# Kernel optimization log

Measured on AMD Instinct MI355X. Metric: run time of the kernel, lower is better.

Reference implementation:

```python
import jax, jax.numpy as jnp
import numpy as np

B, N, DM = 4, 1024, 256
DEPTH, D_STATE, D_CONV, EXPAND = 12, 16, 4, 2
D_INNER = EXPAND * DM
DT_RANK = (DM + 15) // 16
MASKED = 256            # fixed number of masked tokens per row (CLS never masked)
MAX_VIS = N - MASKED    # static visible length -> jit-safe gather/pad
EPS = 1e-5


def setup_inputs() -> dict:
    key = jax.random.key(0)
    ks = jax.random.split(key, 8)
    tokens = jax.random.normal(ks[0], (B, N, DM), jnp.float32)
    # mask: exactly MASKED random positions True per row, among first N-1 (CLS visible)
    def row_mask(k):
        perm = jax.random.permutation(k, N - 1)
        return jnp.zeros((N,), bool).at[perm[:MASKED]].set(True)
    mask = jax.vmap(row_mask)(jax.random.split(ks[1], B))
    sc = 0.02
    L = DEPTH
    in_proj_w = jax.random.normal(ks[2], (L, 2 * D_INNER, DM), jnp.float32) * sc
    conv_w = jax.random.normal(ks[3], (L, D_INNER, D_CONV), jnp.float32) * sc
    conv_b = jnp.zeros((L, D_INNER), jnp.float32)
    x_proj_w = jax.random.normal(ks[4], (L, DT_RANK + 2 * D_STATE, D_INNER), jnp.float32) * sc
    dt_proj_w = jax.random.normal(ks[5], (L, D_INNER, DT_RANK), jnp.float32) * (DT_RANK ** -0.5)
    dt_proj_b = jnp.full((L, D_INNER), float(np.log(np.expm1(0.01))), jnp.float32)  # softplus^-1(0.01)
    A_log = jnp.log(jnp.broadcast_to(jnp.arange(1, D_STATE + 1, dtype=jnp.float32), (L, D_INNER, D_STATE)))
    D_skip = jnp.ones((L, D_INNER), jnp.float32)
    out_proj_w = jax.random.normal(ks[6], (L, DM, D_INNER), jnp.float32) * sc
    norm_w = jnp.ones((L, DM), jnp.float32)
    norm_f_w = jnp.ones((DM,), jnp.float32)
    ln_w = jnp.ones((DM,), jnp.float32)
    ln_b = jnp.zeros((DM,), jnp.float32)
    return dict(tokens=tokens, mask=mask, in_proj_w=in_proj_w, conv_w=conv_w, conv_b=conv_b,
                x_proj_w=x_proj_w, dt_proj_w=dt_proj_w, dt_proj_b=dt_proj_b, A_log=A_log,
                D_skip=D_skip, out_proj_w=out_proj_w, norm_w=norm_w, norm_f_w=norm_f_w,
                ln_w=ln_w, ln_b=ln_b)


def _rmsnorm(x, w):
    return x * jax.lax.rsqrt(jnp.mean(x * x, axis=-1, keepdims=True) + EPS) * w


def _selective_scan(dA, dBu, C):
    # linear recurrence h_t = dA_t * h_{t-1} + dBu_t via associative scan over time
    def comb(l, r):
        return (r[0] * l[0], r[0] * l[1] + r[1])
    _, h = jax.lax.associative_scan(comb, (dA, dBu), axis=1)  # [B,L,d_inner,d_state]
    return jnp.einsum('blds,bls->bld', h, C)


def _mamba(h, p):
    in_w, cw, cb, xw, dtw, dtb, Alog, Dd, ow = p
    L = h.shape[1]
    xz = jnp.einsum('bld,ed->ble', h, in_w)           # [B,L,2*d_inner]
    x, z = jnp.split(xz, 2, axis=-1)
    # causal depthwise conv1d (torch Conv1d, padding=d_conv-1, truncated to L)
    xp = jnp.pad(x, ((0, 0), (D_CONV - 1, 0), (0, 0)))
    x = sum(xp[:, k:k + L, :] * cw[:, k] for k in range(D_CONV)) + cb
    x = jax.nn.silu(x)
    xdbl = jnp.einsum('bld,ed->ble', x, xw)           # [B,L,dt_rank+2*d_state]
    dtr = xdbl[..., :DT_RANK]
    Bm = xdbl[..., DT_RANK:DT_RANK + D_STATE]
    Cm = xdbl[..., DT_RANK + D_STATE:]
    dt = jax.nn.softplus(jnp.einsum('blr,dr->bld', dtr, dtw) + dtb)  # [B,L,d_inner]
    A = -jnp.exp(Alog)                                 # [d_inner,d_state]
    dA = jnp.exp(dt[..., None] * A)                    # [B,L,d_inner,d_state]
    dBu = (dt * x)[..., None] * Bm[:, :, None, :]
    y = _selective_scan(dA, dBu, Cm) + Dd * x
    y = y * jax.nn.silu(z)
    return jnp.einsum('bld,od->blo', y, ow)


def _forward(tokens, mask, in_proj_w, conv_w, conv_b, x_proj_w, dt_proj_w, dt_proj_b,
             A_log, D_skip, out_proj_w, norm_w, norm_f_w, ln_w, ln_b):
    # gather visible tokens, preserving order (stable sort: visible first)
    sort_key = mask.astype(jnp.int32) * N + jnp.arange(N)
    order = jnp.argsort(sort_key, axis=1)[:, :MAX_VIS]           # [B,MAX_VIS]
    vis = jnp.take_along_axis(tokens, order[..., None], axis=1)  # [B,MAX_VIS,DM]

    def step(carry, p):
        hidden, residual = carry
        residual = hidden + residual
        hidden = _mamba(_rmsnorm(residual, p[0]), p[1:])
        return (hidden, residual), None

    layer_params = (norm_w, in_proj_w, conv_w, conv_b, x_proj_w, dt_proj_w, dt_proj_b,
                    A_log, D_skip, out_proj_w)
    (h, r), _ = jax.lax.scan(step, (vis, jnp.zeros_like(vis)), layer_params)
    h = _rmsnorm(h + r, norm_f_w)
    # final nn.LayerNorm
    mu = jnp.mean(h, axis=-1, keepdims=True)
    var = jnp.mean((h - mu) ** 2, axis=-1, keepdims=True)
    h = (h - mu) * jax.lax.rsqrt(var + EPS) * ln_w + ln_b
    return h[:, :-1], h[:, -1]


def reference(tokens, mask, in_proj_w, conv_w, conv_b, x_proj_w, dt_proj_w, dt_proj_b,
              A_log, D_skip, out_proj_w, norm_w, norm_f_w, ln_w, ln_b):
    return _forward(tokens, mask, in_proj_w, conv_w, conv_b, x_proj_w, dt_proj_w, dt_proj_b,
                    A_log, D_skip, out_proj_w, norm_w, norm_f_w, ln_w, ln_b)
```

## Files before the change

kernel.cpp:

```cpp
#include <hip/hip_runtime.h>
#include <stdint.h>

#define B_ 4
#define N_TOK 1024
#define DM 256
#define DEPTH 12
#define DSTATE 16
#define DIN 512
#define LVIS 768
#define MROWS (B_ * LVIS)
#define NCHUNK 64
#define CLEN 12
#define EPS_F 1e-5f
#define YS 520
#define AS_ 264

typedef __attribute__((ext_vector_type(8))) short s8v;
typedef __attribute__((ext_vector_type(4))) float f4v;

__device__ __forceinline__ float bs2f(uint32_t u) {
  uint32_t x = (u & 0xffffu) << 16;
  float f; __builtin_memcpy(&f, &x, 4); return f;
}
__device__ __forceinline__ uint16_t f2b(float f) {
  uint32_t u; __builtin_memcpy(&u, &f, 4);
  return (uint16_t)((u + 0x7fffu + ((u >> 16) & 1u)) >> 16);
}
__device__ __forceinline__ float silu_f(float x) { return x / (1.f + __expf(-x)); }
__device__ __forceinline__ float softplus_f(float x) {
  return fmaxf(x, 0.f) + log1pf(__expf(-fabsf(x)));
}
__device__ __forceinline__ float block_sum256(float v, volatile float* scr) {
  int t = threadIdx.x, lane = t & 63, wid = t >> 6;
#pragma unroll
  for (int o = 32; o > 0; o >>= 1) v += __shfl_down(v, o);
  __syncthreads();
  if (lane == 0) scr[wid] = v;
  __syncthreads();
  return scr[0] + scr[1] + scr[2] + scr[3];
}

__global__ void detect_kernel(const void* mask, const uint32_t* nf, int* flags) {
  __shared__ int cnt[3];
  int t = threadIdx.x;
  if (t < 3) cnt[t] = 0;
  __syncthreads();
  const uint32_t* pi = (const uint32_t*)mask;
  const uint16_t* ph = (const uint16_t*)mask;
  const uint8_t*  pb = (const uint8_t*)mask;
  int c32 = 0, cbf = 0, c8 = 0;
  for (int i = t; i < 1024; i += 256) {
    c32 += (pi[i] != 0u);
    cbf += (ph[i] != 0);
    c8  += (pb[i] != 0);
  }
  atomicAdd(&cnt[0], c32);
  atomicAdd(&cnt[1], cbf);
  atomicAdd(&cnt[2], c8);
  __syncthreads();
  if (t == 0) {
    int f;
    if (cnt[0] == 256) f = 0;
    else if (cnt[1] == 256) f = 2;
    else f = 1;
    flags[0] = f;
    flags[1] = (nf[0] == 0x3F800000u) ? 0 : 1;
  }
}

struct CvtArgs {
  const void* src[13];
  void*       dst[13];
  int         n[13];
  int         isb16[13];
};
__global__ __launch_bounds__(256) void cvt_all_kernel(CvtArgs a, int total,
                                                      const int* __restrict__ flags) {
  int e = blockIdx.x * 256 + threadIdx.x;
  if (e >= total) return;
  int i = 0;
  while (e >= a.n[i]) { e -= a.n[i]; ++i; }
  int srcb16 = flags[1];
  if (a.isb16[i]) {
    uint16_t v = srcb16 ? ((const uint16_t*)a.src[i])[e]
                        : f2b(((const float*)a.src[i])[e]);
    ((uint16_t*)a.dst[i])[e] = v;
  } else {
    float v = srcb16 ? bs2f(((const uint16_t*)a.src[i])[e])
                     : ((const float*)a.src[i])[e];
    ((float*)a.dst[i])[e] = v;
  }
}

__global__ __launch_bounds__(1024) void order_kernel(const void* mask,
                                                     const int* __restrict__ flags,
                                                     int* __restrict__ order) {
  int b = blockIdx.x, i = threadIdx.x;
  int f = flags[0];
  int mv;
  if (f == 0)      mv = (((const uint32_t*)mask)[b * N_TOK + i] != 0u);
  else if (f == 1) mv = (((const uint8_t*)mask)[b * N_TOK + i] != 0);
  else             mv = (((const uint16_t*)mask)[b * N_TOK + i] != 0);
  int vis = !mv;
  unsigned long long mb = __ballot(vis);
  int lane = i & 63, wid = i >> 6;
  int wpre = __popcll(mb & ((1ull << lane) - 1ull));
  __shared__ int wsum[16];
  __shared__ int woff[16];
  if (lane == 0) wsum[wid] = __popcll(mb);
  __syncthreads();
  if (i == 0) { int a = 0; for (int w = 0; w < 16; ++w) { woff[w] = a; a += wsum[w]; } }
  __syncthreads();
  if (vis) {
    int pos = woff[wid] + wpre;
    if (pos < LVIS) order[b * LVIS + pos] = i;
  }
}

__global__ __launch_bounds__(256) void gather_rms_kernel(const void* __restrict__ tokens,
                                                         const int* __restrict__ order,
                                                         const int* __restrict__ flags,
                                                         const float* __restrict__ nw,
                                                         float* __restrict__ residual,
                                                         uint16_t* __restrict__ rmsb16) {
  __shared__ float scr[4];
  int row = blockIdx.x;
  int b = row / LVIS;
  int d = threadIdx.x;
  int idx = order[row];
  size_t src = ((size_t)(b * N_TOK + idx)) * DM + d;
  float v = flags[1] ? bs2f(((const uint16_t*)tokens)[src]) : ((const float*)tokens)[src];
  size_t i = (size_t)row * DM + d;
  residual[i] = v;
  float ss = block_sum256(v * v, scr);
  rmsb16[i] = f2b(v * rsqrtf(ss / DM + EPS_F) * nw[d]);
}

__device__ __forceinline__ size_t cidx(int b, int c, int s, int d) {
  return (((size_t)(b * NCHUNK + c) * 16 + s)) * DIN + d;
}

__global__ __launch_bounds__(1024, 4) void scan1_kernel(
    const uint16_t* __restrict__ rmsb16, const uint16_t* __restrict__ inw,
    const uint16_t* __restrict__ xw,
    const float* __restrict__ cw, const float* __restrict__ cb,
    const float* __restrict__ dtw, const float* __restrict__ dtb,
    const float* __restrict__ Alog,
    uint16_t* __restrict__ xz16, float* __restrict__ hend,
    float* __restrict__ pend, float* __restrict__ xdbl_out) {
  __shared__ uint16_t As[16 * AS_];
  __shared__ uint16_t xzl[16 * YS];
  __shared__ float red[8][768];
  __shared__ float xds[CLEN * 48];
  const int t = threadIdx.x;
  const int wv = t >> 6, lane = t & 63;
  const int lm = lane & 15, lq = lane >> 4;
  const int c = blockIdx.x & (NCHUNK - 1);
  const int b = blockIdx.x >> 6;
  const int rowbase = b * LVIS + c * CLEN;
  if (t < 512) {
    int r = t >> 5, seg = t & 31;
    int grow = rowbase - 3 + r;
    if (grow < 0) grow = 0;
    if (grow > MROWS - 1) grow = MROWS - 1;
    *(uint4*)(As + r * AS_ + seg * 8) =
        *(const uint4*)(rmsb16 + (size_t)grow * DM + seg * 8);
  }
  __syncthreads();
  {
    f4v acc[4];
#pragma unroll
    for (int j = 0; j < 4; ++j) acc[j] = (f4v){0.f, 0.f, 0.f, 0.f};
    for (int k0 = 0; k0 < DM; k0 += 32) {
      s8v a = *(const s8v*)(As + lm * AS_ + k0 + lq * 8);
#pragma unroll
      for (int j = 0; j < 4; ++j) {
        int n = (4 * wv + j) * 16 + lm;
        s8v bw = *(const s8v*)(inw + (size_t)n * DM + k0 + lq * 8);
        acc[j] = __builtin_amdgcn_mfma_f32_16x16x32_bf16(a, bw, acc[j], 0, 0, 0);
      }
    }
#pragma unroll
    for (int j = 0; j < 4; ++j) {
      int col = (4 * wv + j) * 16 + lm;
#pragma unroll
      for (int rr = 0; rr < 4; ++rr) {
        int tr = lq * 4 + rr;
        uint16_t v = f2b(acc[j][rr]);
        if (col < 512) xzl[tr * YS + col] = v;
        if (tr >= 3 && tr < 15)
          xz16[(size_t)(rowbase + tr - 3) * 1024 + col] = v;
      }
    }
  }
  __syncthreads();
  if (wv < 8) {
    f4v acc[3];
#pragma unroll
    for (int j = 0; j < 3; ++j) acc[j] = (f4v){0.f, 0.f, 0.f, 0.f};
    const int l = c * CLEN + lm;
    const bool t3 = l >= 3, t2 = l >= 2, t1 = l >= 1;
#pragma unroll
    for (int ki = 0; ki < 2; ++ki) {
      int kk = wv * 64 + ki * 32 + lq * 8;
      s8v a8 = {0, 0, 0, 0, 0, 0, 0, 0};
      if (lm < CLEN) {
        const s8v zv = {0, 0, 0, 0, 0, 0, 0, 0};
        s8v x0 = *(const s8v*)(xzl + (lm + 3) * YS + kk);
        s8v x1 = t1 ? *(const s8v*)(xzl + (lm + 2) * YS + kk) : zv;
        s8v x2 = t2 ? *(const s8v*)(xzl + (lm + 1) * YS + kk) : zv;
        s8v x3 = t3 ? *(const s8v*)(xzl + (lm + 0) * YS + kk) : zv;
#pragma unroll
        for (int j = 0; j < 8; ++j) {
          int ch = kk + j;
          float4 w = *(const float4*)(cw + ch * 4);
          float a = cb[ch] + bs2f((uint16_t)x3[j]) * w.x +
                    bs2f((uint16_t)x2[j]) * w.y +
                    bs2f((uint16_t)x1[j]) * w.z + bs2f((uint16_t)x0[j]) * w.w;
          a8[j] = (short)f2b(silu_f(a));
        }
      }
#pragma unroll
      for (int j = 0; j < 3; ++j) {
        s8v bb = *(const s8v*)(xw + (size_t)(j * 16 + lm) * DIN + kk);
        acc[j] = __builtin_amdgcn_mfma_f32_16x16x32_bf16(a8, bb, acc[j], 0, 0, 0);
      }
    }
#pragma unroll
    for (int j = 0; j < 3; ++j)
#pragma unroll
      for (int rr = 0; rr < 4; ++rr)
        red[wv][(lq * 4 + rr) * 48 + j * 16 + lm] = acc[j][rr];
  }
  __syncthreads();
  if (t < CLEN * 48) {
    float v = red[0][t] + red[1][t] + red[2][t] + red[3][t] +
              red[4][t] + red[5][t] + red[6][t] + red[7][t];
    xds[t] = v;
    xdbl_out[(size_t)(rowbase + t / 48) * 48 + (t % 48)] = v;
  }
  __syncthreads();
  if (t < DIN) {
    const int d = t;
    float A[16], dw[16];
    {
      const float4* ap = (const float4*)(Alog + (size_t)d * 16);
      const float4* wp = (const float4*)(dtw + (size_t)d * 16);
#pragma unroll
      for (int q = 0; q < 4; ++q) {
        float4 a4 = ap[q], w4 = wp[q];
        A[4 * q + 0] = -__expf(a4.x); A[4 * q + 1] = -__expf(a4.y);
        A[4 * q + 2] = -__expf(a4.z); A[4 * q + 3] = -__expf(a4.w);
        dw[4 * q + 0] = w4.x; dw[4 * q + 1] = w4.y;
        dw[4 * q + 2] = w4.z; dw[4 * q + 3] = w4.w;
      }
    }
    float dtbv = dtb[d], cbv = cb[d];
    float4 cwv = *(const float4*)(cw + d * 4);
    float w3 = 0.f, w2 = 0.f, w1 = 0.f;
    if (c > 0) {
      w3 = bs2f(xzl[0 * YS + d]);
      w2 = bs2f(xzl[1 * YS + d]);
      w1 = bs2f(xzl[2 * YS + d]);
    }
    float h[16], p[16];
#pragma unroll
    for (int s = 0; s < 16; ++s) { h[s] = 0.f; p[s] = 1.f; }
    for (int l = 0; l < CLEN; ++l) {
      float xn = bs2f(xzl[(l + 3) * YS + d]);
      float xv = silu_f(cbv + w3 * cwv.x + w2 * cwv.y + w1 * cwv.z + xn * cwv.w);
      w3 = w2; w2 = w1; w1 = xn;
      const float* xd = xds + l * 48;
      float dtraw = dtbv;
#pragma unroll
      for (int q = 0; q < 16; ++q) dtraw += xd[q] * dw[q];
      float dtv = softplus_f(dtraw);
      float dtx = dtv * xv;
#pragma unroll
      for (int s = 0; s < 16; ++s) {
        float dA = __expf(dtv * A[s]);
        h[s] = dA * h[s] + dtx * xd[16 + s];
        p[s] *= dA;
      }
    }
#pragma unroll
    for (int s = 0; s < 16; ++s) {
      hend[cidx(b, c, s, d)] = h[s];
      pend[cidx(b, c, s, d)] = p[s];
    }
  }
}

__global__ __launch_bounds__(256) void scan2_kernel(const float* __restrict__ hend,
                                                    const float* __restrict__ pend,
                                                    float* __restrict__ hin) {
  __shared__ float sP[4 * 64];
  __shared__ float sE[4 * 64];
  int t = threadIdx.x;
  int w = t >> 6, lane = t & 63;
  int chain = blockIdx.x * 64 + lane;
  int d = chain & (DIN - 1);
  int s = (chain >> 9) & 15;
  int b = chain >> 13;
  float P = 1.f, E = 0.f;
  float pr[16], hr[16];
#pragma unroll
  for (int i = 0; i < 16; ++i) {
    size_t idx = cidx(b, w * 16 + i, s, d);
    float pv = pend[idx], ev = hend[idx];
    pr[i] = pv; hr[i] = ev;
    E = pv * E + ev;
    P *= pv;
  }
  sP[w * 64 + lane] = P;
  sE[w * 64 + lane] = E;
  __syncthreads();
  float hc = 0.f;
#pragma unroll
  for (int j = 0; j < 3; ++j)
    if (j < w) hc = sP[j * 64 + lane] * hc + sE[j * 64 + lane];
#pragma unroll
  for (int i = 0; i < 16; ++i) {
    hin[cidx(b, w * 16 + i, s, d)] = hc;
    hc = pr[i] * hc + hr[i];
  }
}

__global__ __launch_bounds__(1024, 4) void scan3_fused_kernel(
    const uint16_t* __restrict__ xz16, const float* __restrict__ xdbl,
    const float* __restrict__ dtw, const float* __restrict__ dtb,
    const float* __restrict__ cw, const float* __restrict__ cb,
    const float* __restrict__ Alog, const float* __restrict__ Dskip,
    const float* __restrict__ hin, const uint16_t* __restrict__ W,
    const float* __restrict__ nw, float* __restrict__ residual,
    uint16_t* __restrict__ rmsb16) {
  __shared__ float xds[CLEN * 48];
  __shared__ uint16_t yml[16 * YS];
  __shared__ float part[16][16];
  __shared__ float scale[16];
  const int t = threadIdx.x;
  const int c = blockIdx.x & (NCHUNK - 1);
  const int b = blockIdx.x >> 6;
  const int rowbase = b * LVIS + c * CLEN;
  if (t < CLEN * 48)
    xds[t] = xdbl[(size_t)(rowbase + t / 48) * 48 + (t % 48)];
  for (int e = t; e < 4 * 512; e += 1024)
    yml[(12 + (e >> 9)) * YS + (e & 511)] = 0;
  __syncthreads();
  if (t < DIN) {
    const int d = t;
    float A[16], dw[16];
    {
      const float4* ap = (const float4*)(Alog + (size_t)d * 16);
      const float4* wp = (const float4*)(dtw + (size_t)d * 16);
#pragma unroll
      for (int q = 0; q < 4; ++q) {
        float4 a4 = ap[q], w4 = wp[q];
        A[4 * q + 0] = -__expf(a4.x); A[4 * q + 1] = -__expf(a4.y);
        A[4 * q + 2] = -__expf(a4.z); A[4 * q + 3] = -__expf(a4.w);
        dw[4 * q + 0] = w4.x; dw[4 * q + 1] = w4.y;
        dw[4 * q + 2] = w4.z; dw[4 * q + 3] = w4.w;
      }
    }
    float h[16];
#pragma unroll
    for (int s = 0; s < 16; ++s) h[s] = hin[cidx(b, c, s, d)];
    float dtbv = dtb[d], cbv = cb[d], Dv = Dskip[d];
    float4 cwv = *(const float4*)(cw + d * 4);
    float w3 = 0.f, w2 = 0.f, w1 = 0.f;
    if (c > 0) {
      w3 = bs2f(xz16[(size_t)(rowbase - 3) * 1024 + d]);
      w2 = bs2f(xz16[(size_t)(rowbase - 2) * 1024 + d]);
      w1 = bs2f(xz16[(size_t)(rowbase - 1) * 1024 + d]);
    }
    for (int l = 0; l < CLEN; ++l) {
      int row = rowbase + l;
      float xn = bs2f(xz16[(size_t)row * 1024 + d]);
      float xv = silu_f(cbv + w3 * cwv.x + w2 * cwv.y + w1 * cwv.z + xn * cwv.w);
      w3 = w2; w2 = w1; w1 = xn;
      const float* xd = xds + l * 48;
      float dtraw = dtbv;
#pragma unroll
      for (int q = 0; q < 16; ++q) dtraw += xd[q] * dw[q];
      float dtv = softplus_f(dtraw);
      float dtx = dtv * xv;
      float y = 0.f;
#pragma unroll
      for (int s = 0; s < 16; ++s) {
        float dA = __expf(dtv * A[s]);
        h[s] = dA * h[s] + dtx * xd[16 + s];
        y += h[s] * xd[32 + s];
      }
      float zv = bs2f(xz16[(size_t)row * 1024 + 512 + d]);
      yml[l * YS + d] = f2b((y + Dv * xv) * silu_f(zv));
    }
  }
  __syncthreads();
  {
    const int wv = t >> 6, lane = t & 63;
    const int lm = lane & 15, lq = lane >> 4;
    f4v acc = (f4v){0.f, 0.f, 0.f, 0.f};
    for (int k0 = 0; k0 < DIN; k0 += 32) {
      s8v a = *(const s8v*)(yml + lm * YS + k0 + lq * 8);
      int n = wv * 16 + lm;
      s8v bf = *(const s8v*)(W + (size_t)n * DIN + k0 + lq * 8);
      acc = __builtin_amdgcn_mfma_f32_16x16x32_bf16(a, bf, acc, 0, 0, 0);
    }
    float vv[4];
    float sum[4] = {0.f, 0.f, 0.f, 0.f};
#pragma unroll
    for (int rr = 0; rr < 4; ++rr) {
      int row = lq * 4 + rr;
      if (row < CLEN) {
        int col = wv * 16 + lm;
        float v = acc[rr] + residual[(size_t)(rowbase + row) * DM + col];
        vv[rr] = v;
        sum[rr] += v * v;
      }
    }
#pragma unroll
    for (int rr = 0; rr < 4; ++rr) {
#pragma unroll
      for (int o = 1; o < 16; o <<= 1) sum[rr] += __shfl_xor(sum[rr], o);
    }
    if (lm == 0) {
#pragma unroll
      for (int rr = 0; rr < 4; ++rr) {
        int row = lq * 4 + rr;
        if (row < 16) part[row][wv] = sum[rr];
      }
    }
    __syncthreads();
    if (t < CLEN) {
      float s = 0.f;
#pragma unroll
      for (int w = 0; w < 16; ++w) s += part[t][w];
      scale[t] = rsqrtf(s / DM + EPS_F);
    }
    __syncthreads();
#pragma unroll
    for (int rr = 0; rr < 4; ++rr) {
      int row = lq * 4 + rr;
      if (row < CLEN) {
        float sc = scale[row];
        int col = wv * 16 + lm;
        float v = vv[rr];
        size_t oi = (size_t)(rowbase + row) * DM + col;
        residual[oi] = v;
        rmsb16[oi] = f2b(v * sc * nw[col]);
      }
    }
  }
}

__global__ __launch_bounds__(256) void final_kernel(const float* __restrict__ residual,
                                                    const float* __restrict__ nfw,
                                                    const float* __restrict__ lnw,
                                                    const float* __restrict__ lnb,
                                                    const int* __restrict__ flags,
                                                    void* __restrict__ out) {
  __shared__ float scr[4];
  int row = blockIdx.x, d = threadIdx.x;
  size_t i = (size_t)row * DM + d;
  float v = residual[i];
  float ss = block_sum256(v * v, scr);
  float h = v * rsqrtf(ss / DM + EPS_F) * nfw[d];
  float mu = block_sum256(h, scr) / DM;
  float dv = h - mu;
  float var = block_sum256(dv * dv, scr) / DM;
  float o = dv * rsqrtf(var + EPS_F) * lnw[d] + lnb[d];
  int b = row / LVIS, l = row % LVIS;
  size_t oi = (l < LVIS - 1)
                ? ((size_t)(b * (LVIS - 1) + l) * DM + d)
                : ((size_t)B_ * (LVIS - 1) * DM + (size_t)b * DM + d);
  if (flags[1]) ((uint16_t*)out)[oi] = f2b(o);
  else          ((float*)out)[oi] = o;
}

extern "C" void kernel_launch(void* const* d_in, const int* in_sizes, int n_in,
                              void* d_out, int out_size, void* d_ws, size_t ws_size,
                              hipStream_t stream) {
  char* ws = (char*)d_ws;
  size_t off = 0;
  auto alloc = [&](size_t bytes) -> void* {
    void* p = ws + off;
    off += (bytes + 255) & ~(size_t)255;
    return p;
  };
  const int f32_idx[10] = {3, 4, 6, 7, 8, 9, 11, 12, 13, 14};
  const int b16_idx[3]  = {2, 5, 10};
  float*    f32c[15] = {nullptr};
  uint16_t* b16c[15] = {nullptr};
  for (int j = 0; j < 10; ++j) {
    int i = f32_idx[j];
    f32c[i] = (float*)alloc((size_t)in_sizes[i] * 4);
  }
  for (int j = 0; j < 3; ++j) {
    int i = b16_idx[j];
    b16c[i] = (uint16_t*)alloc((size_t)in_sizes[i] * 2);
  }
  float*    residual = (float*)alloc((size_t)MROWS * DM * 4);
  uint16_t* rmsb16   = (uint16_t*)alloc((size_t)MROWS * DM * 2);
  uint16_t* xz16     = (uint16_t*)alloc((size_t)MROWS * 1024 * 2);
  float*    xdbl     = (float*)alloc((size_t)MROWS * 48 * 4);
  float*    hend     = (float*)alloc((size_t)B_ * NCHUNK * DIN * 16 * 4);
  float*    pend     = (float*)alloc((size_t)B_ * NCHUNK * DIN * 16 * 4);
  float*    hin      = (float*)alloc((size_t)B_ * NCHUNK * DIN * 16 * 4);
  int*      order    = (int*)alloc((size_t)B_ * LVIS * 4);
  int*      flags    = (int*)alloc(256);

  detect_kernel<<<1, 256, 0, stream>>>(d_in[1], (const uint32_t*)d_in[12], flags);

  CvtArgs ca;
  int total = 0, slot = 0;
  for (int j = 0; j < 3; ++j) {
    int i = b16_idx[j];
    ca.src[slot] = d_in[i]; ca.dst[slot] = b16c[i];
    ca.n[slot] = in_sizes[i]; ca.isb16[slot] = 1;
    total += in_sizes[i]; ++slot;
  }
  for (int j = 0; j < 10; ++j) {
    int i = f32_idx[j];
    ca.src[slot] = d_in[i]; ca.dst[slot] = f32c[i];
    ca.n[slot] = in_sizes[i]; ca.isb16[slot] = 0;
    total += in_sizes[i]; ++slot;
  }
  cvt_all_kernel<<<(total + 255) / 256, 256, 0, stream>>>(ca, total, flags);

  const uint16_t* in_w   = b16c[2];
  const float*    conv_w = f32c[3];
  const float*    conv_b = f32c[4];
  const uint16_t* x_w    = b16c[5];
  const float*    dt_w   = f32c[6];
  const float*    dt_b   = f32c[7];
  const float*    A_log  = f32c[8];
  const float*    D_skip = f32c[9];
  const uint16_t* out_w  = b16c[10];
  const float*    norm_w = f32c[11];
  const float*    norm_f = f32c[12];
  const float*    ln_w   = f32c[13];
  const float*    ln_b   = f32c[14];

  order_kernel<<<B_, 1024, 0, stream>>>(d_in[1], flags, order);
  gather_rms_kernel<<<MROWS, 256, 0, stream>>>(d_in[0], order, flags, norm_w,
                                               residual, rmsb16);

  for (int L = 0; L < DEPTH; ++L) {
    scan1_kernel<<<B_ * NCHUNK, 1024, 0, stream>>>(
        rmsb16, in_w + (size_t)L * 1024 * DM, x_w + (size_t)L * 48 * DIN,
        conv_w + (size_t)L * DIN * 4, conv_b + (size_t)L * DIN,
        dt_w + (size_t)L * DIN * 16, dt_b + (size_t)L * DIN,
        A_log + (size_t)L * DIN * 16, xz16, hend, pend, xdbl);
    scan2_kernel<<<(B_ * 16 * DIN * 4) / 256, 256, 0, stream>>>(hend, pend, hin);
    int Lnext = (L + 1 < DEPTH) ? (L + 1) : L;
    scan3_fused_kernel<<<B_ * NCHUNK, 1024, 0, stream>>>(
        xz16, xdbl, dt_w + (size_t)L * DIN * 16, dt_b + (size_t)L * DIN,
        conv_w + (size_t)L * DIN * 4, conv_b + (size_t)L * DIN,
        A_log + (size_t)L * DIN * 16, D_skip + (size_t)L * DIN, hin,
        out_w + (size_t)L * DM * DIN, norm_w + (size_t)Lnext * DM,
        residual, rmsb16);
  }

  final_kernel<<<MROWS, 256, 0, stream>>>(residual, norm_f, ln_w, ln_b,
                                          flags, d_out);
}
```

Baseline: 939.3 us.

## Stage xz tiles in LDS for coalesced stores/loads and atomic x_proj reduction

In scan1, the full 1024-wide in_proj output tile is staged in shared memory. Idle waves 8-15 then write it to global memory with 16-byte vector stores while waves 0-7 run the x_proj MFMA. The 8-way partial-sum buffer and one barrier are replaced by LDS atomicAdd into a single reduction buffer. In scan3, the chunk's xz rows are bulk-loaded into LDS with vector loads instead of strided per-thread global reads inside the scan loop. This adds LDS footprint and atomic contention, which may reduce occupancy.

```diff
diff --git a/kernel.cpp b/kernel.cpp
--- a/kernel.cpp
+++ b/kernel.cpp
@@ -12,6 +12,7 @@
 #define NCHUNK 64
 #define CLEN 12
 #define EPS_F 1e-5f
+#define XS2 1040
 #define YS 520
 #define AS_ 264
 
@@ -149,9 +150,8 @@
     uint16_t* __restrict__ xz16, float* __restrict__ hend,
     float* __restrict__ pend, float* __restrict__ xdbl_out) {
   __shared__ uint16_t As[16 * AS_];
-  __shared__ uint16_t xzl[16 * YS];
-  __shared__ float red[8][768];
-  __shared__ float xds[CLEN * 48];
+  __shared__ uint16_t xzf[16 * XS2];
+  __shared__ float redf[768];
   const int t = threadIdx.x;
   const int wv = t >> 6, lane = t & 63;
   const int lm = lane & 15, lq = lane >> 4;
@@ -166,6 +166,7 @@
     *(uint4*)(As + r * AS_ + seg * 8) =
         *(const uint4*)(rmsb16 + (size_t)grow * DM + seg * 8);
   }
+  if (t < 768) redf[t] = 0.f;
   __syncthreads();
   {
     f4v acc[4];
@@ -186,15 +187,18 @@
 #pragma unroll
       for (int rr = 0; rr < 4; ++rr) {
         int tr = lq * 4 + rr;
-        uint16_t v = f2b(acc[j][rr]);
-        if (col < 512) xzl[tr * YS + col] = v;
-        if (tr >= 3 && tr < 15)
-          xz16[(size_t)(rowbase + tr - 3) * 1024 + col] = v;
-      }
-    }
-  }
-  __syncthreads();
-  if (wv < 8) {
+        xzf[tr * XS2 + col] = f2b(acc[j][rr]);
+      }
+    }
+  }
+  __syncthreads();
+  if (wv >= 8) {
+    for (int e = t - 512; e < 12 * 128; e += 512) {
+      int r = e >> 7, q = e & 127;
+      *(uint4*)(xz16 + (size_t)(rowbase + r) * 1024 + q * 8) =
+          *(const uint4*)(xzf + (3 + r) * XS2 + q * 8);
+    }
+  } else {
     f4v acc[3];
 #pragma unroll
     for (int j = 0; j < 3; ++j) acc[j] = (f4v){0.f, 0.f, 0.f, 0.f};
@@ -206,10 +210,10 @@
       s8v a8 = {0, 0, 0, 0, 0, 0, 0, 0};
       if (lm < CLEN) {
         const s8v zv = {0, 0, 0, 0, 0, 0, 0, 0};
-        s8v x0 = *(const s8v*)(xzl + (lm + 3) * YS + kk);
-        s8v x1 = t1 ? *(const s8v*)(xzl + (lm + 2) * YS + kk) : zv;
-        s8v x2 = t2 ? *(const s8v*)(xzl + (lm + 1) * YS + kk) : zv;
-        s8v x3 = t3 ? *(const s8v*)(xzl + (lm + 0) * YS + kk) : zv;
+        s8v x0 = *(const s8v*)(xzf + (lm + 3) * XS2 + kk);
+        s8v x1 = t1 ? *(const s8v*)(xzf + (lm + 2) * XS2 + kk) : zv;
+        s8v x2 = t2 ? *(const s8v*)(xzf + (lm + 1) * XS2 + kk) : zv;
+        s8v x3 = t3 ? *(const s8v*)(xzf + (lm + 0) * XS2 + kk) : zv;
 #pragma unroll
         for (int j = 0; j < 8; ++j) {
           int ch = kk + j;
@@ -230,16 +234,11 @@
     for (int j = 0; j < 3; ++j)
 #pragma unroll
       for (int rr = 0; rr < 4; ++rr)
-        red[wv][(lq * 4 + rr) * 48 + j * 16 + lm] = acc[j][rr];
-  }
-  __syncthreads();
-  if (t < CLEN * 48) {
-    float v = red[0][t] + red[1][t] + red[2][t] + red[3][t] +
-              red[4][t] + red[5][t] + red[6][t] + red[7][t];
-    xds[t] = v;
-    xdbl_out[(size_t)(rowbase + t / 48) * 48 + (t % 48)] = v;
-  }
-  __syncthreads();
+        atomicAdd(&redf[(lq * 4 + rr) * 48 + j * 16 + lm], acc[j][rr]);
+  }
+  __syncthreads();
+  if (t < CLEN * 48)
+    xdbl_out[(size_t)(rowbase + t / 48) * 48 + (t % 48)] = redf[t];
   if (t < DIN) {
     const int d = t;
     float A[16], dw[16];
@@ -259,18 +258,18 @@
     float4 cwv = *(const float4*)(cw + d * 4);
     float w3 = 0.f, w2 = 0.f, w1 = 0.f;
     if (c > 0) {
-      w3 = bs2f(xzl[0 * YS + d]);
-      w2 = bs2f(xzl[1 * YS + d]);
-      w1 = bs2f(xzl[2 * YS + d]);
+      w3 = bs2f(xzf[0 * XS2 + d]);
+      w2 = bs2f(xzf[1 * XS2 + d]);
+      w1 = bs2f(xzf[2 * XS2 + d]);
     }
     float h[16], p[16];
 #pragma unroll
     for (int s = 0; s < 16; ++s) { h[s] = 0.f; p[s] = 1.f; }
     for (int l = 0; l < CLEN; ++l) {
-      float xn = bs2f(xzl[(l + 3) * YS + d]);
+      float xn = bs2f(xzf[(l + 3) * XS2 + d]);
       float xv = silu_f(cbv + w3 * cwv.x + w2 * cwv.y + w1 * cwv.z + xn * cwv.w);
       w3 = w2; w2 = w1; w1 = xn;
-      const float* xd = xds + l * 48;
+      const float* xd = redf + l * 48;
       float dtraw = dtbv;
 #pragma unroll
       for (int q = 0; q < 16; ++q) dtraw += xd[q] * dw[q];
@@ -334,6 +333,7 @@
     const float* __restrict__ hin, const uint16_t* __restrict__ W,
     const float* __restrict__ nw, float* __restrict__ residual,
     uint16_t* __restrict__ rmsb16) {
+  __shared__ uint16_t xzst[CLEN * XS2];
   __shared__ float xds[CLEN * 48];
   __shared__ uint16_t yml[16 * YS];
   __shared__ float part[16][16];
@@ -342,6 +342,11 @@
   const int c = blockIdx.x & (NCHUNK - 1);
   const int b = blockIdx.x >> 6;
   const int rowbase = b * LVIS + c * CLEN;
+  for (int e = t; e < 12 * 128; e += 1024) {
+    int r = e >> 7, q = e & 127;
+    *(uint4*)(xzst + r * XS2 + q * 8) =
+        *(const uint4*)(xz16 + (size_t)(rowbase + r) * 1024 + q * 8);
+  }
   if (t < CLEN * 48)
     xds[t] = xdbl[(size_t)(rowbase + t / 48) * 48 + (t % 48)];
   for (int e = t; e < 4 * 512; e += 1024)
@@ -374,8 +379,7 @@
       w1 = bs2f(xz16[(size_t)(rowbase - 1) * 1024 + d]);
     }
     for (int l = 0; l < CLEN; ++l) {
-      int row = rowbase + l;
-      float xn = bs2f(xz16[(size_t)row * 1024 + d]);
+      float xn = bs2f(xzst[l * XS2 + d]);
       float xv = silu_f(cbv + w3 * cwv.x + w2 * cwv.y + w1 * cwv.z + xn * cwv.w);
       w3 = w2; w2 = w1; w1 = xn;
       const float* xd = xds + l * 48;
@@ -391,7 +395,7 @@
         h[s] = dA * h[s] + dtx * xd[16 + s];
         y += h[s] * xd[32 + s];
       }
-      float zv = bs2f(xz16[(size_t)row * 1024 + 512 + d]);
+      float zv = bs2f(xzst[l * XS2 + 512 + d]);
       yml[l * YS + d] = f2b((y + Dv * xv) * silu_f(zv));
     }
   }
```

After: 1.007 ms. +7.2%, slower.

## Halve scan chunk length and split state dimension across thread pairs

Applied to the files above, without the earlier changes.

Doubles the number of sequence chunks (128 chunks of 6 tokens) so twice as many blocks run per layer. Inside the chunked scan kernels, each channel's 16 states are now split across two threads, which combine partial outputs with a lane shuffle, so all 1024 threads do scan work. The chunk-combine kernel is widened to 8 waves per block to match. The cost is that in-projection MFMA tiles now carry only 6 useful rows out of 16 plus 3 halo rows, so GEMM work and weight reloads per token roughly double, and hend/pend traffic doubles.

```diff
diff --git a/kernel.cpp b/kernel.cpp
--- a/kernel.cpp
+++ b/kernel.cpp
@@ -9,8 +9,8 @@
 #define DIN 512
 #define LVIS 768
 #define MROWS (B_ * LVIS)
-#define NCHUNK 64
-#define CLEN 12
+#define NCHUNK 128
+#define CLEN 6
 #define EPS_F 1e-5f
 #define YS 520
 #define AS_ 264
@@ -140,7 +140,7 @@
   return (((size_t)(b * NCHUNK + c) * 16 + s)) * DIN + d;
 }
 
-__global__ __launch_bounds__(1024, 4) void scan1_kernel(
+__global__ __launch_bounds__(1024, 8) void scan1_kernel(
     const uint16_t* __restrict__ rmsb16, const uint16_t* __restrict__ inw,
     const uint16_t* __restrict__ xw,
     const float* __restrict__ cw, const float* __restrict__ cb,
@@ -156,7 +156,7 @@
   const int wv = t >> 6, lane = t & 63;
   const int lm = lane & 15, lq = lane >> 4;
   const int c = blockIdx.x & (NCHUNK - 1);
-  const int b = blockIdx.x >> 6;
+  const int b = blockIdx.x >> 7;
   const int rowbase = b * LVIS + c * CLEN;
   if (t < 512) {
     int r = t >> 5, seg = t & 31;
@@ -188,7 +188,7 @@
         int tr = lq * 4 + rr;
         uint16_t v = f2b(acc[j][rr]);
         if (col < 512) xzl[tr * YS + col] = v;
-        if (tr >= 3 && tr < 15)
+        if (tr >= 3 && tr < 3 + CLEN)
           xz16[(size_t)(rowbase + tr - 3) * 1024 + col] = v;
       }
     }
@@ -240,17 +240,22 @@
     xdbl_out[(size_t)(rowbase + t / 48) * 48 + (t % 48)] = v;
   }
   __syncthreads();
-  if (t < DIN) {
-    const int d = t;
-    float A[16], dw[16];
+  {
+    const int d = t >> 1;
+    const int s0 = (t & 1) * 8;
+    float A[8], dw[16];
     {
-      const float4* ap = (const float4*)(Alog + (size_t)d * 16);
+      const float4* ap = (const float4*)(Alog + (size_t)d * 16 + s0);
       const float4* wp = (const float4*)(dtw + (size_t)d * 16);
 #pragma unroll
-      for (int q = 0; q < 4; ++q) {
-        float4 a4 = ap[q], w4 = wp[q];
+      for (int q = 0; q < 2; ++q) {
+        float4 a4 = ap[q];
         A[4 * q + 0] = -__expf(a4.x); A[4 * q + 1] = -__expf(a4.y);
         A[4 * q + 2] = -__expf(a4.z); A[4 * q + 3] = -__expf(a4.w);
+      }
+#pragma unroll
+      for (int q = 0; q < 4; ++q) {
+        float4 w4 = wp[q];
         dw[4 * q + 0] = w4.x; dw[4 * q + 1] = w4.y;
         dw[4 * q + 2] = w4.z; dw[4 * q + 3] = w4.w;
       }
@@ -263,9 +268,9 @@
       w2 = bs2f(xzl[1 * YS + d]);
       w1 = bs2f(xzl[2 * YS + d]);
     }
-    float h[16], p[16];
-#pragma unroll
-    for (int s = 0; s < 16; ++s) { h[s] = 0.f; p[s] = 1.f; }
+    float h[8], p[8];
+#pragma unroll
+    for (int i = 0; i < 8; ++i) { h[i] = 0.f; p[i] = 1.f; }
     for (int l = 0; l < CLEN; ++l) {
       float xn = bs2f(xzl[(l + 3) * YS + d]);
       float xv = silu_f(cbv + w3 * cwv.x + w2 * cwv.y + w1 * cwv.z + xn * cwv.w);
@@ -277,25 +282,25 @@
       float dtv = softplus_f(dtraw);
       float dtx = dtv * xv;
 #pragma unroll
-      for (int s = 0; s < 16; ++s) {
-        float dA = __expf(dtv * A[s]);
-        h[s] = dA * h[s] + dtx * xd[16 + s];
-        p[s] *= dA;
-      }
-    }
-#pragma unroll
-    for (int s = 0; s < 16; ++s) {
-      hend[cidx(b, c, s, d)] = h[s];
-      pend[cidx(b, c, s, d)] = p[s];
-    }
-  }
-}
-
-__global__ __launch_bounds__(256) void scan2_kernel(const float* __restrict__ hend,
+      for (int i = 0; i < 8; ++i) {
+        float dA = __expf(dtv * A[i]);
+        h[i] = dA * h[i] + dtx * xd[16 + s0 + i];
+        p[i] *= dA;
+      }
+    }
+#pragma unroll
+    for (int i = 0; i < 8; ++i) {
+      hend[cidx(b, c, s0 + i, d)] = h[i];
+      pend[cidx(b, c, s0 + i, d)] = p[i];
+    }
+  }
+}
+
+__global__ __launch_bounds__(512) void scan2_kernel(const float* __restrict__ hend,
                                                     const float* __restrict__ pend,
                                                     float* __restrict__ hin) {
-  __shared__ float sP[4 * 64];
-  __shared__ float sE[4 * 64];
+  __shared__ float sP[8 * 64];
+  __shared__ float sE[8 * 64];
   int t = threadIdx.x;
   int w = t >> 6, lane = t & 63;
   int chain = blockIdx.x * 64 + lane;
@@ -317,7 +322,7 @@
   __syncthreads();
   float hc = 0.f;
 #pragma unroll
-  for (int j = 0; j < 3; ++j)
+  for (int j = 0; j < 7; ++j)
     if (j < w) hc = sP[j * 64 + lane] * hc + sE[j * 64 + lane];
 #pragma unroll
   for (int i = 0; i < 16; ++i) {
@@ -326,7 +331,7 @@
   }
 }
 
-__global__ __launch_bounds__(1024, 4) void scan3_fused_kernel(
+__global__ __launch_bounds__(1024, 8) void scan3_fused_kernel(
     const uint16_t* __restrict__ xz16, const float* __restrict__ xdbl,
     const float* __restrict__ dtw, const float* __restrict__ dtb,
     const float* __restrict__ cw, const float* __restrict__ cb,
@@ -340,31 +345,36 @@
   __shared__ float scale[16];
   const int t = threadIdx.x;
   const int c = blockIdx.x & (NCHUNK - 1);
-  const int b = blockIdx.x >> 6;
+  const int b = blockIdx.x >> 7;
   const int rowbase = b * LVIS + c * CLEN;
   if (t < CLEN * 48)
     xds[t] = xdbl[(size_t)(rowbase + t / 48) * 48 + (t % 48)];
-  for (int e = t; e < 4 * 512; e += 1024)
-    yml[(12 + (e >> 9)) * YS + (e & 511)] = 0;
-  __syncthreads();
-  if (t < DIN) {
-    const int d = t;
-    float A[16], dw[16];
+  for (int e = t; e < (16 - CLEN) * 512; e += 1024)
+    yml[(CLEN + (e >> 9)) * YS + (e & 511)] = 0;
+  __syncthreads();
+  {
+    const int d = t >> 1;
+    const int s0 = (t & 1) * 8;
+    float A[8], dw[16];
     {
-      const float4* ap = (const float4*)(Alog + (size_t)d * 16);
+      const float4* ap = (const float4*)(Alog + (size_t)d * 16 + s0);
       const float4* wp = (const float4*)(dtw + (size_t)d * 16);
 #pragma unroll
-      for (int q = 0; q < 4; ++q) {
-        float4 a4 = ap[q], w4 = wp[q];
+      for (int q = 0; q < 2; ++q) {
+        float4 a4 = ap[q];
         A[4 * q + 0] = -__expf(a4.x); A[4 * q + 1] = -__expf(a4.y);
         A[4 * q + 2] = -__expf(a4.z); A[4 * q + 3] = -__expf(a4.w);
+      }
+#pragma unroll
+      for (int q = 0; q < 4; ++q) {
+        float4 w4 = wp[q];
         dw[4 * q + 0] = w4.x; dw[4 * q + 1] = w4.y;
         dw[4 * q + 2] = w4.z; dw[4 * q + 3] = w4.w;
       }
     }
-    float h[16];
-#pragma unroll
-    for (int s = 0; s < 16; ++s) h[s] = hin[cidx(b, c, s, d)];
+    float h[8];
+#pragma unroll
+    for (int i = 0; i < 8; ++i) h[i] = hin[cidx(b, c, s0 + i, d)];
     float dtbv = dtb[d], cbv = cb[d], Dv = Dskip[d];
     float4 cwv = *(const float4*)(cw + d * 4);
     float w3 = 0.f, w2 = 0.f, w1 = 0.f;
@@ -386,13 +396,15 @@
       float dtx = dtv * xv;
       float y = 0.f;
 #pragma unroll
-      for (int s = 0; s < 16; ++s) {
-        float dA = __expf(dtv * A[s]);
-        h[s] = dA * h[s] + dtx * xd[16 + s];
-        y += h[s] * xd[32 + s];
-      }
+      for (int i = 0; i < 8; ++i) {
+        float dA = __expf(dtv * A[i]);
+        h[i] = dA * h[i] + dtx * xd[16 + s0 + i];
+        y += h[i] * xd[32 + s0 + i];
+      }
+      y += __shfl_xor(y, 1);
       float zv = bs2f(xz16[(size_t)row * 1024 + 512 + d]);
-      yml[l * YS + d] = f2b((y + Dv * xv) * silu_f(zv));
+      if (!(t & 1))
+        yml[l * YS + d] = f2b((y + Dv * xv) * silu_f(zv));
     }
   }
   __syncthreads();
@@ -551,7 +563,7 @@
         conv_w + (size_t)L * DIN * 4, conv_b + (size_t)L * DIN,
         dt_w + (size_t)L * DIN * 16, dt_b + (size_t)L * DIN,
         A_log + (size_t)L * DIN * 16, xz16, hend, pend, xdbl);
-    scan2_kernel<<<(B_ * 16 * DIN * 4) / 256, 256, 0, stream>>>(hend, pend, hin);
+    scan2_kernel<<<(B_ * 16 * DIN) / 64, 512, 0, stream>>>(hend, pend, hin);
     int Lnext = (L + 1 < DEPTH) ? (L + 1) : L;
     scan3_fused_kernel<<<B_ * NCHUNK, 1024, 0, stream>>>(
         xz16, xdbl, dt_w + (size_t)L * DIN * 16, dt_b + (size_t)L * DIN,
```

New measurement: 1.471 ms. +56.6%, slower.

## Compute local scan outputs in pass one and apply carry-in correction in pass three

Applied to the files above, without the earlier changes.

The first chunk-scan pass now also emits the chunk-local output y (including the D skip term) and the running sum of dt per position. The third pass therefore no longer replays the recurrence: it adds the contribution of the incoming state as sum_s C_s*h_in_s*exp(A_s*S). This removes the second sequential 16-state recurrence and its convolution and softplus recomputation, at the cost of writing and reading two extra fp32 [rows x 512] buffers per layer. Silu, softplus and exp also switch to raw v_exp/v_log/v_rcp instructions with log2e-prescaled A, and the chunk decay product is computed as one exp2 of A times the dt sum.

```diff
diff --git a/kernel.cpp b/kernel.cpp
--- a/kernel.cpp
+++ b/kernel.cpp
@@ -14,6 +14,8 @@
 #define EPS_F 1e-5f
 #define YS 520
 #define AS_ 264
+#define LOG2E 1.4426950408889634f
+#define LN2   0.6931471805599453f
 
 typedef __attribute__((ext_vector_type(8))) short s8v;
 typedef __attribute__((ext_vector_type(4))) float f4v;
@@ -26,9 +28,21 @@
   uint32_t u; __builtin_memcpy(&u, &f, 4);
   return (uint16_t)((u + 0x7fffu + ((u >> 16) & 1u)) >> 16);
 }
-__device__ __forceinline__ float silu_f(float x) { return x / (1.f + __expf(-x)); }
+__device__ __forceinline__ float exp2_f(float x) {
+  float r; asm("v_exp_f32 %0, %1" : "=v"(r) : "v"(x)); return r;
+}
+__device__ __forceinline__ float log2_f(float x) {
+  float r; asm("v_log_f32 %0, %1" : "=v"(r) : "v"(x)); return r;
+}
+__device__ __forceinline__ float rcp_f(float x) {
+  float r; asm("v_rcp_f32 %0, %1" : "=v"(r) : "v"(x)); return r;
+}
+__device__ __forceinline__ float silu_f(float x) {
+  return x * rcp_f(1.f + exp2_f(-x * LOG2E));
+}
 __device__ __forceinline__ float softplus_f(float x) {
-  return fmaxf(x, 0.f) + log1pf(__expf(-fabsf(x)));
+  float t = exp2_f(-fabsf(x) * LOG2E);
+  return fmaxf(x, 0.f) + log2_f(1.f + t) * LN2;
 }
 __device__ __forceinline__ float block_sum256(float v, volatile float* scr) {
   int t = threadIdx.x, lane = t & 63, wid = t >> 6;
@@ -145,9 +159,10 @@
     const uint16_t* __restrict__ xw,
     const float* __restrict__ cw, const float* __restrict__ cb,
     const float* __restrict__ dtw, const float* __restrict__ dtb,
-    const float* __restrict__ Alog,
+    const float* __restrict__ Alog, const float* __restrict__ Dsk,
     uint16_t* __restrict__ xz16, float* __restrict__ hend,
-    float* __restrict__ pend, float* __restrict__ xdbl_out) {
+    float* __restrict__ pend, float* __restrict__ xdbl_out,
+    float* __restrict__ yloc, float* __restrict__ Ssum) {
   __shared__ uint16_t As[16 * AS_];
   __shared__ uint16_t xzl[16 * YS];
   __shared__ float red[8][768];
@@ -242,20 +257,22 @@
   __syncthreads();
   if (t < DIN) {
     const int d = t;
-    float A[16], dw[16];
+    float A2[16], dw[16];
     {
       const float4* ap = (const float4*)(Alog + (size_t)d * 16);
       const float4* wp = (const float4*)(dtw + (size_t)d * 16);
 #pragma unroll
       for (int q = 0; q < 4; ++q) {
         float4 a4 = ap[q], w4 = wp[q];
-        A[4 * q + 0] = -__expf(a4.x); A[4 * q + 1] = -__expf(a4.y);
-        A[4 * q + 2] = -__expf(a4.z); A[4 * q + 3] = -__expf(a4.w);
+        A2[4 * q + 0] = -__expf(a4.x) * LOG2E;
+        A2[4 * q + 1] = -__expf(a4.y) * LOG2E;
+        A2[4 * q + 2] = -__expf(a4.z) * LOG2E;
+        A2[4 * q + 3] = -__expf(a4.w) * LOG2E;
         dw[4 * q + 0] = w4.x; dw[4 * q + 1] = w4.y;
         dw[4 * q + 2] = w4.z; dw[4 * q + 3] = w4.w;
       }
     }
-    float dtbv = dtb[d], cbv = cb[d];
+    float dtbv = dtb[d], cbv = cb[d], Dv = Dsk[d];
     float4 cwv = *(const float4*)(cw + d * 4);
     float w3 = 0.f, w2 = 0.f, w1 = 0.f;
     if (c > 0) {
@@ -263,9 +280,10 @@
       w2 = bs2f(xzl[1 * YS + d]);
       w1 = bs2f(xzl[2 * YS + d]);
     }
-    float h[16], p[16];
-#pragma unroll
-    for (int s = 0; s < 16; ++s) { h[s] = 0.f; p[s] = 1.f; }
+    float h[16];
+#pragma unroll
+    for (int s = 0; s < 16; ++s) h[s] = 0.f;
+    float S = 0.f;
     for (int l = 0; l < CLEN; ++l) {
       float xn = bs2f(xzl[(l + 3) * YS + d]);
       float xv = silu_f(cbv + w3 * cwv.x + w2 * cwv.y + w1 * cwv.z + xn * cwv.w);
@@ -276,17 +294,22 @@
       for (int q = 0; q < 16; ++q) dtraw += xd[q] * dw[q];
       float dtv = softplus_f(dtraw);
       float dtx = dtv * xv;
+      S += dtv;
+      float y = 0.f;
 #pragma unroll
       for (int s = 0; s < 16; ++s) {
-        float dA = __expf(dtv * A[s]);
+        float dA = exp2_f(dtv * A2[s]);
         h[s] = dA * h[s] + dtx * xd[16 + s];
-        p[s] *= dA;
-      }
+        y += h[s] * xd[32 + s];
+      }
+      size_t oi = (size_t)(rowbase + l) * DIN + d;
+      yloc[oi] = y + Dv * xv;
+      Ssum[oi] = S;
     }
 #pragma unroll
     for (int s = 0; s < 16; ++s) {
       hend[cidx(b, c, s, d)] = h[s];
-      pend[cidx(b, c, s, d)] = p[s];
+      pend[cidx(b, c, s, d)] = exp2_f(A2[s] * S);
     }
   }
 }
@@ -328,12 +351,10 @@
 
 __global__ __launch_bounds__(1024, 4) void scan3_fused_kernel(
     const uint16_t* __restrict__ xz16, const float* __restrict__ xdbl,
-    const float* __restrict__ dtw, const float* __restrict__ dtb,
-    const float* __restrict__ cw, const float* __restrict__ cb,
-    const float* __restrict__ Alog, const float* __restrict__ Dskip,
-    const float* __restrict__ hin, const uint16_t* __restrict__ W,
-    const float* __restrict__ nw, float* __restrict__ residual,
-    uint16_t* __restrict__ rmsb16) {
+    const float* __restrict__ Alog, const float* __restrict__ hin,
+    const float* __restrict__ yloc, const float* __restrict__ Ssum,
+    const uint16_t* __restrict__ W, const float* __restrict__ nw,
+    float* __restrict__ residual, uint16_t* __restrict__ rmsb16) {
   __shared__ float xds[CLEN * 48];
   __shared__ uint16_t yml[16 * YS];
   __shared__ float part[16][16];
@@ -349,50 +370,33 @@
   __syncthreads();
   if (t < DIN) {
     const int d = t;
-    float A[16], dw[16];
+    float A2[16];
     {
       const float4* ap = (const float4*)(Alog + (size_t)d * 16);
-      const float4* wp = (const float4*)(dtw + (size_t)d * 16);
 #pragma unroll
       for (int q = 0; q < 4; ++q) {
-        float4 a4 = ap[q], w4 = wp[q];
-        A[4 * q + 0] = -__expf(a4.x); A[4 * q + 1] = -__expf(a4.y);
-        A[4 * q + 2] = -__expf(a4.z); A[4 * q + 3] = -__expf(a4.w);
-        dw[4 * q + 0] = w4.x; dw[4 * q + 1] = w4.y;
-        dw[4 * q + 2] = w4.z; dw[4 * q + 3] = w4.w;
-      }
-    }
-    float h[16];
-#pragma unroll
-    for (int s = 0; s < 16; ++s) h[s] = hin[cidx(b, c, s, d)];
-    float dtbv = dtb[d], cbv = cb[d], Dv = Dskip[d];
-    float4 cwv = *(const float4*)(cw + d * 4);
-    float w3 = 0.f, w2 = 0.f, w1 = 0.f;
-    if (c > 0) {
-      w3 = bs2f(xz16[(size_t)(rowbase - 3) * 1024 + d]);
-      w2 = bs2f(xz16[(size_t)(rowbase - 2) * 1024 + d]);
-      w1 = bs2f(xz16[(size_t)(rowbase - 1) * 1024 + d]);
-    }
+        float4 a4 = ap[q];
+        A2[4 * q + 0] = -__expf(a4.x) * LOG2E;
+        A2[4 * q + 1] = -__expf(a4.y) * LOG2E;
+        A2[4 * q + 2] = -__expf(a4.z) * LOG2E;
+        A2[4 * q + 3] = -__expf(a4.w) * LOG2E;
+      }
+    }
+    float chin[16];
+#pragma unroll
+    for (int s = 0; s < 16; ++s) chin[s] = hin[cidx(b, c, s, d)];
     for (int l = 0; l < CLEN; ++l) {
       int row = rowbase + l;
-      float xn = bs2f(xz16[(size_t)row * 1024 + d]);
-      float xv = silu_f(cbv + w3 * cwv.x + w2 * cwv.y + w1 * cwv.z + xn * cwv.w);
-      w3 = w2; w2 = w1; w1 = xn;
+      size_t oi = (size_t)row * DIN + d;
+      float S = Ssum[oi];
+      float yl = yloc[oi];
       const float* xd = xds + l * 48;
-      float dtraw = dtbv;
-#pragma unroll
-      for (int q = 0; q < 16; ++q) dtraw += xd[q] * dw[q];
-      float dtv = softplus_f(dtraw);
-      float dtx = dtv * xv;
-      float y = 0.f;
-#pragma unroll
-      for (int s = 0; s < 16; ++s) {
-        float dA = __expf(dtv * A[s]);
-        h[s] = dA * h[s] + dtx * xd[16 + s];
-        y += h[s] * xd[32 + s];
-      }
+      float carry = 0.f;
+#pragma unroll
+      for (int s = 0; s < 16; ++s)
+        carry += xd[32 + s] * chin[s] * exp2_f(A2[s] * S);
       float zv = bs2f(xz16[(size_t)row * 1024 + 512 + d]);
-      yml[l * YS + d] = f2b((y + Dv * xv) * silu_f(zv));
+      yml[l * YS + d] = f2b((yl + carry) * silu_f(zv));
     }
   }
   __syncthreads();
@@ -506,6 +510,8 @@
   float*    hend     = (float*)alloc((size_t)B_ * NCHUNK * DIN * 16 * 4);
   float*    pend     = (float*)alloc((size_t)B_ * NCHUNK * DIN * 16 * 4);
   float*    hin      = (float*)alloc((size_t)B_ * NCHUNK * DIN * 16 * 4);
+  float*    yloc     = (float*)alloc((size_t)MROWS * DIN * 4);
+  float*    Ssum     = (float*)alloc((size_t)MROWS * DIN * 4);
   int*      order    = (int*)alloc((size_t)B_ * LVIS * 4);
   int*      flags    = (int*)alloc(256);
 
@@ -550,13 +556,12 @@
         rmsb16, in_w + (size_t)L * 1024 * DM, x_w + (size_t)L * 48 * DIN,
         conv_w + (size_t)L * DIN * 4, conv_b + (size_t)L * DIN,
         dt_w + (size_t)L * DIN * 16, dt_b + (size_t)L * DIN,
-        A_log + (size_t)L * DIN * 16, xz16, hend, pend, xdbl);
+        A_log + (size_t)L * DIN * 16, D_skip + (size_t)L * DIN,
+        xz16, hend, pend, xdbl, yloc, Ssum);
     scan2_kernel<<<(B_ * 16 * DIN * 4) / 256, 256, 0, stream>>>(hend, pend, hin);
     int Lnext = (L + 1 < DEPTH) ? (L + 1) : L;
     scan3_fused_kernel<<<B_ * NCHUNK, 1024, 0, stream>>>(
-        xz16, xdbl, dt_w + (size_t)L * DIN * 16, dt_b + (size_t)L * DIN,
-        conv_w + (size_t)L * DIN * 4, conv_b + (size_t)L * DIN,
-        A_log + (size_t)L * DIN * 16, D_skip + (size_t)L * DIN, hin,
+        xz16, xdbl, A_log + (size_t)L * DIN * 16, hin, yloc, Ssum,
         out_w + (size_t)L * DM * DIN, norm_w + (size_t)Lnext * DM,
         residual, rmsb16);
   }
```

Result: faster. 798.7 us (-15.0%).
